# Optimization experiments

Hardware: AMD Instinct MI355X
Metric: run time of the kernel (lower is better)

## Reference

```python
import jax, jax.numpy as jnp
import numpy as np

N_NODES = 50000
N_EDGES = 1600000
D_FEAT = 512
FILTERS = 256
NUM_CLASSES = 16


def setup_inputs() -> dict:
    key = jax.random.key(0)
    k = jax.random.split(key, 6)
    x = jax.random.normal(k[0], (N_NODES, D_FEAT), dtype=jnp.float32)
    W1 = jax.random.normal(k[1], (D_FEAT, FILTERS), dtype=jnp.float32) * (1.0 / np.sqrt(D_FEAT))
    W2 = jax.random.normal(k[2], (FILTERS, NUM_CLASSES), dtype=jnp.float32) * (1.0 / np.sqrt(FILTERS))
    edge_weight = jax.random.uniform(k[3], (N_EDGES,), dtype=jnp.float32)
    edge_src = jax.random.randint(k[4], (N_EDGES,), 0, N_NODES, dtype=jnp.int32)
    edge_dst = jax.random.randint(k[5], (N_EDGES,), 0, N_NODES, dtype=jnp.int32)
    return {"x": x, "W1": W1, "W2": W2, "edge_weight": edge_weight,
            "edge_src": edge_src, "edge_dst": edge_dst}


def _propagate(h, edge_src, edge_dst, edge_weight):
    # sparse A @ h: out[dst] += w * h[src]
    msgs = edge_weight[:, None] * h[edge_src]          # [E, F]
    return jax.ops.segment_sum(msgs, edge_dst, num_segments=N_NODES)


def reference(x, W1, W2, edge_weight, edge_src, edge_dst):
    # Dropout layers are identity at inference (training=False).
    # Layer 1: relu(A @ (X @ W1))
    h = jax.nn.relu(_propagate(x @ W1, edge_src, edge_dst, edge_weight))
    # Layer 2: softmax(A @ (H @ W2))
    logits = _propagate(h @ W2, edge_src, edge_dst, edge_weight)
    return jax.nn.softmax(logits, axis=-1)
```

## Files before the change

### kernel.cpp

```cpp
#include <hip/hip_runtime.h>

#define N_NODES 50000
#define N_EDGES 1600000
#define D_FEAT 512
#define FILTERS 256
#define NUM_CLASSES 16
#define NXCD 8

typedef __bf16 bf16x8 __attribute__((ext_vector_type(8)));
typedef float f32x4 __attribute__((ext_vector_type(4)));
typedef _Float16 half4 __attribute__((ext_vector_type(4)));
typedef _Float16 f16x8 __attribute__((ext_vector_type(8)));

#define GLOAD_LDS16(g, l)                                                  \
  __builtin_amdgcn_global_load_lds(                                        \
      (const __attribute__((address_space(1))) unsigned int*)(g),          \
      (__attribute__((address_space(3))) unsigned int*)(l), 16, 0, 0)

__global__ __launch_bounds__(256) void split_w1_kernel(
    const float* __restrict__ W1, __bf16* __restrict__ Wth,
    __bf16* __restrict__ Wtl) {
  const int idx = blockIdx.x * 256 + threadIdx.x;
  const int k = idx >> 8;
  const int n = idx & 255;
  const float v = W1[idx];
  const __bf16 h = (__bf16)v;
  const __bf16 l = (__bf16)(v - (float)h);
  Wth[n * D_FEAT + k] = h;
  Wtl[n * D_FEAT + k] = l;
}

__global__ __launch_bounds__(256) void hist8_kernel(
    const int* __restrict__ edst, int* __restrict__ deg8) {
  const int e = blockIdx.x * 256 + threadIdx.x;
  if (e >= N_EDGES) return;
  const int x = blockIdx.x & (NXCD - 1);
  atomicAdd(&deg8[x * N_NODES + edst[e]], 1);
}

#define SCAN_NB 196
__global__ __launch_bounds__(256) void scan_blocks_kernel(
    const int* __restrict__ deg8, int* __restrict__ row_ptr,
    int* __restrict__ bsum) {
  __shared__ int s[256];
  const int i = blockIdx.x * 256 + threadIdx.x;
  int v = 0;
  if (i < N_NODES) {
#pragma unroll
    for (int x = 0; x < NXCD; ++x) v += deg8[x * N_NODES + i];
  }
  s[threadIdx.x] = v;
  __syncthreads();
  for (int off = 1; off < 256; off <<= 1) {
    const int t = (threadIdx.x >= off) ? s[threadIdx.x - off] : 0;
    __syncthreads();
    s[threadIdx.x] += t;
    __syncthreads();
  }
  if (i < N_NODES) row_ptr[i] = s[threadIdx.x] - v;
  if (threadIdx.x == 255) bsum[blockIdx.x] = s[255];
}

__global__ __launch_bounds__(256) void scan_sums_kernel(int* __restrict__ bsum) {
  __shared__ int s[256];
  const int v = (threadIdx.x < SCAN_NB) ? bsum[threadIdx.x] : 0;
  s[threadIdx.x] = v;
  __syncthreads();
  for (int off = 1; off < 256; off <<= 1) {
    const int t = (threadIdx.x >= off) ? s[threadIdx.x - off] : 0;
    __syncthreads();
    s[threadIdx.x] += t;
    __syncthreads();
  }
  if (threadIdx.x < SCAN_NB) bsum[threadIdx.x] = s[threadIdx.x] - v;
}

__global__ __launch_bounds__(256) void scan_add_cursor8_kernel(
    int* __restrict__ row_ptr, const int* __restrict__ bsum,
    const int* __restrict__ deg8, int* __restrict__ cursor8) {
  const int i = blockIdx.x * 256 + threadIdx.x;
  if (i < N_NODES) {
    int run = row_ptr[i] + bsum[blockIdx.x];
    row_ptr[i] = run;
#pragma unroll
    for (int x = 0; x < NXCD; ++x) {
      cursor8[x * N_NODES + i] = run;
      run += deg8[x * N_NODES + i];
    }
  }
  if (i == 0) row_ptr[N_NODES] = N_EDGES;
}

__global__ __launch_bounds__(256) void fill8_kernel(
    const int* __restrict__ esrc, const int* __restrict__ edst,
    const float* __restrict__ ew, int* __restrict__ cursor8,
    int4* __restrict__ meta) {
  const int e = blockIdx.x * 256 + threadIdx.x;
  if (e >= N_EDGES) return;
  const int x = blockIdx.x & (NXCD - 1);
  const int d = edst[e];
  const int pos = atomicAdd(&cursor8[x * N_NODES + d], 1);
  meta[pos] = make_int4(esrc[e], __float_as_int(ew[e]), d, 0);
}

__global__ __launch_bounds__(256) void gemm1_mfma_kernel(
    const float* __restrict__ A, const __bf16* __restrict__ Bh,
    const __bf16* __restrict__ Bl, _Float16* __restrict__ C) {
  const int K = D_FEAT;
  __shared__ __bf16 sAh[128 * 32];
  __shared__ __bf16 sAl[128 * 32];
  __shared__ __bf16 sBh[128 * 32];
  __shared__ __bf16 sBl[128 * 32];

  const int tid = threadIdx.x;
  const int wave = tid >> 6;
  const int lane = tid & 63;
  const int wm = (wave >> 1) * 64;
  const int wn = (wave & 1) * 64;
  const int m0 = blockIdx.x * 128;
  const int n0 = blockIdx.y * 128;

  const int arow = tid >> 1;
  const int aks = (tid & 1) * 16;
  int am = m0 + arow;
  if (am >= N_NODES) am = N_NODES - 1;
  const float* aptr = A + (size_t)am * K + aks;

  const int lr = lane >> 2;
  const int lc = (lane & 3) * 8;
  const int fm = lane & 15;
  const int fq = lane >> 4;

  f32x4 acc[4][4] = {};

  for (int k0 = 0; k0 < K; k0 += 32) {
    const float4* ap = (const float4*)(aptr + k0);
    const float4 a0 = ap[0], a1 = ap[1], a2 = ap[2], a3 = ap[3];

    __syncthreads();

#pragma unroll
    for (int i = 0; i < 2; ++i) {
      const int row = wave * 32 + i * 16;
      GLOAD_LDS16(Bh + (size_t)(n0 + row + lr) * K + k0 + lc, sBh + row * 32);
      GLOAD_LDS16(Bl + (size_t)(n0 + row + lr) * K + k0 + lc, sBl + row * 32);
    }

    float va[16] = {a0.x, a0.y, a0.z, a0.w, a1.x, a1.y, a1.z, a1.w,
                    a2.x, a2.y, a2.z, a2.w, a3.x, a3.y, a3.z, a3.w};
    __bf16 hh[16], ll[16];
#pragma unroll
    for (int i = 0; i < 16; ++i) {
      const __bf16 h = (__bf16)va[i];
      hh[i] = h;
      ll[i] = (__bf16)(va[i] - (float)h);
    }
    *(bf16x8*)(sAh + arow * 32 + aks) = *(bf16x8*)&hh[0];
    *(bf16x8*)(sAh + arow * 32 + aks + 8) = *(bf16x8*)&hh[8];
    *(bf16x8*)(sAl + arow * 32 + aks) = *(bf16x8*)&ll[0];
    *(bf16x8*)(sAl + arow * 32 + aks + 8) = *(bf16x8*)&ll[8];

    __syncthreads();

    bf16x8 fah[4], fal[4], fbh[4], fbl[4];
#pragma unroll
    for (int t = 0; t < 4; ++t) {
      const int moff = (wm + t * 16 + fm) * 32 + fq * 8;
      fah[t] = *(const bf16x8*)(sAh + moff);
      fal[t] = *(const bf16x8*)(sAl + moff);
      const int noff = (wn + t * 16 + fm) * 32 + fq * 8;
      fbh[t] = *(const bf16x8*)(sBh + noff);
      fbl[t] = *(const bf16x8*)(sBl + noff);
    }
#pragma unroll
    for (int i = 0; i < 4; ++i)
#pragma unroll
      for (int j = 0; j < 4; ++j)
        acc[i][j] = __builtin_amdgcn_mfma_f32_16x16x32_bf16(fah[i], fbh[j],
                                                            acc[i][j], 0, 0, 0);
#pragma unroll
    for (int i = 0; i < 4; ++i)
#pragma unroll
      for (int j = 0; j < 4; ++j)
        acc[i][j] = __builtin_amdgcn_mfma_f32_16x16x32_bf16(fah[i], fbl[j],
                                                            acc[i][j], 0, 0, 0);
#pragma unroll
    for (int i = 0; i < 4; ++i)
#pragma unroll
      for (int j = 0; j < 4; ++j)
        acc[i][j] = __builtin_amdgcn_mfma_f32_16x16x32_bf16(fal[i], fbh[j],
                                                            acc[i][j], 0, 0, 0);
  }

#pragma unroll
  for (int ti = 0; ti < 4; ++ti) {
#pragma unroll
    for (int r = 0; r < 4; ++r) {
      const int m = m0 + wm + ti * 16 + fq * 4 + r;
      if (m < N_NODES) {
#pragma unroll
        for (int tj = 0; tj < 4; ++tj) {
          const int n = n0 + wn + tj * 16 + fm;
          C[(size_t)m * FILTERS + n] = (_Float16)acc[ti][tj][r];
        }
      }
    }
  }
}

__global__ __launch_bounds__(256) void gather1_gemm2_kernel(
    const _Float16* __restrict__ xw1, const int* __restrict__ row_ptr,
    const int4* __restrict__ meta, const float* __restrict__ W2,
    _Float16* __restrict__ h2) {
  __shared__ float red[4][16][17];
  const int wave = threadIdx.x >> 6;
  const int lane = threadIdx.x & 63;
  const int node = blockIdx.x * 4 + wave;
  const int beg = row_ptr[node];
  const int end = row_ptr[node + 1];

  float acc[4] = {};
  const half4* __restrict__ xw1v = (const half4*)xw1;

  for (int c0 = beg; c0 < end; c0 += 64) {
    const int cnt = min(64, end - c0);
    const int4 mv = meta[c0 + ((lane < cnt) ? lane : 0)];

    for (int j = 0; j < cnt; j += 8) {
      int srcs[8];
      float ws[8];
#pragma unroll
      for (int u = 0; u < 8; ++u) {
        const int live = (j + u < cnt);
        const int l = live ? (j + u) : 0;
        srcs[u] = __builtin_amdgcn_readlane(mv.x, l);
        const int wb = __builtin_amdgcn_readlane(mv.y, l);
        ws[u] = live ? __int_as_float(wb) : 0.f;
      }
      half4 v[8];
#pragma unroll
      for (int u = 0; u < 8; ++u)
        v[u] = xw1v[(unsigned)srcs[u] * 64u + (unsigned)lane];
#pragma unroll
      for (int u = 0; u < 8; ++u)
#pragma unroll
        for (int i = 0; i < 4; ++i)
          acc[i] = fmaf(ws[u], (float)v[u][i], acc[i]);
    }
  }

  float r[4];
#pragma unroll
  for (int i = 0; i < 4; ++i) r[i] = fmaxf(acc[i], 0.f);

  float p[16] = {};
#pragma unroll
  for (int j = 0; j < 4; ++j) {
    const float4* wr = (const float4*)(W2 + (size_t)(lane * 4 + j) * NUM_CLASSES);
#pragma unroll
    for (int c4 = 0; c4 < 4; ++c4) {
      const float4 wv = wr[c4];
      p[c4 * 4 + 0] = fmaf(r[j], wv.x, p[c4 * 4 + 0]);
      p[c4 * 4 + 1] = fmaf(r[j], wv.y, p[c4 * 4 + 1]);
      p[c4 * 4 + 2] = fmaf(r[j], wv.z, p[c4 * 4 + 2]);
      p[c4 * 4 + 3] = fmaf(r[j], wv.w, p[c4 * 4 + 3]);
    }
  }

#pragma unroll
  for (int off = 32; off >= 16; off >>= 1)
#pragma unroll
    for (int i = 0; i < 16; ++i) p[i] += __shfl_xor(p[i], off, 64);

  if (lane < 16) {
#pragma unroll
    for (int i = 0; i < 16; ++i) red[wave][lane][i] = p[i];
  }
  if (lane < 16) {
    float sum = 0.f;
#pragma unroll
    for (int i = 0; i < 16; ++i) sum += red[wave][i][lane];
    h2[(size_t)node * NUM_CLASSES + lane] = (_Float16)sum;
  }
}

__global__ __launch_bounds__(256) void gather2_mfma_kernel(
    const _Float16* __restrict__ h2, const int* __restrict__ row_ptr,
    const int4* __restrict__ meta, float* __restrict__ out) {
  __shared__ _Float16 lds[4][16][72];
  const int wave = threadIdx.x >> 6;
  const int lane = threadIdx.x & 63;
  const int tile = blockIdx.x * 4 + wave;
  if (tile >= N_NODES / 16) return;
  const int t0 = tile * 16;
  const int beg = row_ptr[t0];
  const int end = row_ptr[t0 + 16];

  const int cls = lane & 15;
  const int kq = lane >> 4;
  const int erow = lane >> 1;
  const int part = lane & 1;

  f32x4 acc = {0.f, 0.f, 0.f, 0.f};
  _Float16* myl = &lds[wave][0][0];

  if (beg < end) {
    const int last = end - 1;
    int e = beg + lane;
    int4 m = meta[(e <= last) ? e : last];
    float wv = (e <= last) ? __int_as_float(m.y) : 0.f;

    for (int c0 = beg; c0 < end; c0 += 64) {
      int4 mn = m;
      float wn = 0.f;
      const int c1 = c0 + 64;
      if (c1 < end) {
        const int en = c1 + lane;
        mn = meta[(en <= last) ? en : last];
        wn = (en <= last) ? __int_as_float(mn.y) : 0.f;
      }

      const int se0 = __shfl(m.x, erow, 64);
      const int se1 = __shfl(m.x, 32 + erow, 64);
      const f16x8 r0 =
          *(const f16x8*)(h2 + (size_t)se0 * NUM_CLASSES + part * 8);
      const f16x8 r1 =
          *(const f16x8*)(h2 + (size_t)se1 * NUM_CLASSES + part * 8);

      f16x8 a0, a1;
#pragma unroll
      for (int j = 0; j < 8; ++j) {
        const int ei = kq * 8 + j;
        const int d0 = __shfl(m.z, ei, 64) - t0;
        const float w0 = __shfl(wv, ei, 64);
        a0[j] = (d0 == cls) ? (_Float16)w0 : (_Float16)0.f;
        const int d1 = __shfl(m.z, 32 + ei, 64) - t0;
        const float w1 = __shfl(wv, 32 + ei, 64);
        a1[j] = (d1 == cls) ? (_Float16)w1 : (_Float16)0.f;
      }

#pragma unroll
      for (int j = 0; j < 8; ++j) myl[(part * 8 + j) * 72 + erow] = r0[j];
#pragma unroll
      for (int j = 0; j < 8; ++j) myl[(part * 8 + j) * 72 + 32 + erow] = r1[j];

      const f16x8 b0 = *(const f16x8*)(myl + cls * 72 + kq * 8);
      const f16x8 b1 = *(const f16x8*)(myl + cls * 72 + 32 + kq * 8);

      acc = __builtin_amdgcn_mfma_f32_16x16x32_f16(a0, b0, acc, 0, 0, 0);
      acc = __builtin_amdgcn_mfma_f32_16x16x32_f16(a1, b1, acc, 0, 0, 0);

      m = mn;
      wv = wn;
    }
  }

#pragma unroll
  for (int r = 0; r < 4; ++r) {
    const float a = acc[r];
    float mx = a;
#pragma unroll
    for (int off = 8; off >= 1; off >>= 1)
      mx = fmaxf(mx, __shfl_xor(mx, off, 16));
    const float ex = __expf(a - mx);
    float sm = ex;
#pragma unroll
    for (int off = 8; off >= 1; off >>= 1) sm += __shfl_xor(sm, off, 16);
    out[(size_t)(t0 + kq * 4 + r) * NUM_CLASSES + cls] = ex / sm;
  }
}

extern "C" void kernel_launch(void* const* d_in, const int* in_sizes, int n_in,
                              void* d_out, int out_size, void* d_ws,
                              size_t ws_size, hipStream_t stream) {
  const float* x = (const float*)d_in[0];
  const float* W1 = (const float*)d_in[1];
  const float* W2 = (const float*)d_in[2];
  const float* ew = (const float*)d_in[3];
  const int* esrc = (const int*)d_in[4];
  const int* edst = (const int*)d_in[5];
  float* out = (float*)d_out;

  _Float16* xw1 = (_Float16*)d_ws;
  _Float16* h2 = xw1 + (size_t)N_NODES * FILTERS;
  int* row_ptr = (int*)(h2 + (size_t)N_NODES * NUM_CLASSES);
  int* deg8 = row_ptr + (N_NODES + 1);
  int* cursor8 = deg8 + NXCD * N_NODES;
  int4* meta = (int4*)(((uintptr_t)(cursor8 + NXCD * N_NODES) + 15) &
                       ~(uintptr_t)15);
  __bf16* w1th = (__bf16*)(meta + N_EDGES);
  __bf16* w1tl = w1th + D_FEAT * FILTERS;
  int* bsum = (int*)(w1tl + D_FEAT * FILTERS);

  hipMemsetAsync(deg8, 0, NXCD * N_NODES * sizeof(int), stream);
  hist8_kernel<<<(N_EDGES + 255) / 256, 256, 0, stream>>>(edst, deg8);
  scan_blocks_kernel<<<SCAN_NB, 256, 0, stream>>>(deg8, row_ptr, bsum);
  scan_sums_kernel<<<1, 256, 0, stream>>>(bsum);
  scan_add_cursor8_kernel<<<SCAN_NB, 256, 0, stream>>>(row_ptr, bsum, deg8,
                                                       cursor8);
  fill8_kernel<<<(N_EDGES + 255) / 256, 256, 0, stream>>>(esrc, edst, ew,
                                                          cursor8, meta);

  split_w1_kernel<<<(D_FEAT * FILTERS) / 256, 256, 0, stream>>>(W1, w1th, w1tl);
  dim3 g1((N_NODES + 127) / 128, FILTERS / 128);
  gemm1_mfma_kernel<<<g1, 256, 0, stream>>>(x, w1th, w1tl, xw1);

  gather1_gemm2_kernel<<<N_NODES / 4, 256, 0, stream>>>(xw1, row_ptr, meta, W2,
                                                        h2);

  gather2_mfma_kernel<<<(N_NODES / 16 + 3) / 4, 256, 0, stream>>>(h2, row_ptr,
                                                                  meta, out);
}
```

Measured before the change: 555.8 us.

## Pack edge metadata into 8 bytes and fold small prep kernels

Edge metadata shrinks from an int4 (src, weight, dst, pad) to a uint2. The source index sits in the low 16 bits, the destination's position within its 16-node tile in bits 16-19, and the weight in the second word. This halves metadata traffic in the fill and both gather kernels. The W1 bf16 hi/lo split moves into the block-scan kernel. The separate scan-of-sums kernel is replaced by each block reducing the preceding block sums itself, which removes two launches. The packing relies on node indices fitting in 16 bits.

```diff
diff --git a/kernel.cpp b/kernel.cpp
--- a/kernel.cpp
+++ b/kernel.cpp
@@ -17,19 +17,6 @@
       (const __attribute__((address_space(1))) unsigned int*)(g),          \
       (__attribute__((address_space(3))) unsigned int*)(l), 16, 0, 0)
 
-__global__ __launch_bounds__(256) void split_w1_kernel(
-    const float* __restrict__ W1, __bf16* __restrict__ Wth,
-    __bf16* __restrict__ Wtl) {
-  const int idx = blockIdx.x * 256 + threadIdx.x;
-  const int k = idx >> 8;
-  const int n = idx & 255;
-  const float v = W1[idx];
-  const __bf16 h = (__bf16)v;
-  const __bf16 l = (__bf16)(v - (float)h);
-  Wth[n * D_FEAT + k] = h;
-  Wtl[n * D_FEAT + k] = l;
-}
-
 __global__ __launch_bounds__(256) void hist8_kernel(
     const int* __restrict__ edst, int* __restrict__ deg8) {
   const int e = blockIdx.x * 256 + threadIdx.x;
@@ -41,9 +28,20 @@
 #define SCAN_NB 196
 __global__ __launch_bounds__(256) void scan_blocks_kernel(
     const int* __restrict__ deg8, int* __restrict__ row_ptr,
-    int* __restrict__ bsum) {
+    int* __restrict__ bsum, const float* __restrict__ W1,
+    __bf16* __restrict__ Wth, __bf16* __restrict__ Wtl) {
+  const int gtid = blockIdx.x * 256 + threadIdx.x;
+  for (int i = gtid; i < D_FEAT * FILTERS; i += SCAN_NB * 256) {
+    const float v = W1[i];
+    const int k = i >> 8;
+    const int n = i & 255;
+    const __bf16 h = (__bf16)v;
+    Wth[n * D_FEAT + k] = h;
+    Wtl[n * D_FEAT + k] = (__bf16)(v - (float)h);
+  }
+
   __shared__ int s[256];
-  const int i = blockIdx.x * 256 + threadIdx.x;
+  const int i = gtid;
   int v = 0;
   if (i < N_NODES) {
 #pragma unroll
@@ -61,26 +59,22 @@
   if (threadIdx.x == 255) bsum[blockIdx.x] = s[255];
 }
 
-__global__ __launch_bounds__(256) void scan_sums_kernel(int* __restrict__ bsum) {
-  __shared__ int s[256];
-  const int v = (threadIdx.x < SCAN_NB) ? bsum[threadIdx.x] : 0;
-  s[threadIdx.x] = v;
-  __syncthreads();
-  for (int off = 1; off < 256; off <<= 1) {
-    const int t = (threadIdx.x >= off) ? s[threadIdx.x - off] : 0;
-    __syncthreads();
-    s[threadIdx.x] += t;
-    __syncthreads();
-  }
-  if (threadIdx.x < SCAN_NB) bsum[threadIdx.x] = s[threadIdx.x] - v;
-}
-
 __global__ __launch_bounds__(256) void scan_add_cursor8_kernel(
     int* __restrict__ row_ptr, const int* __restrict__ bsum,
     const int* __restrict__ deg8, int* __restrict__ cursor8) {
+  __shared__ int wsum[4];
+  const int lane = threadIdx.x & 63;
+  const int wave = threadIdx.x >> 6;
+  int v = (threadIdx.x < blockIdx.x) ? bsum[threadIdx.x] : 0;
+#pragma unroll
+  for (int off = 32; off >= 1; off >>= 1) v += __shfl_xor(v, off, 64);
+  if (lane == 0) wsum[wave] = v;
+  __syncthreads();
+  const int boff = wsum[0] + wsum[1] + wsum[2] + wsum[3];
+
   const int i = blockIdx.x * 256 + threadIdx.x;
   if (i < N_NODES) {
-    int run = row_ptr[i] + bsum[blockIdx.x];
+    int run = row_ptr[i] + boff;
     row_ptr[i] = run;
 #pragma unroll
     for (int x = 0; x < NXCD; ++x) {
@@ -94,13 +88,14 @@
 __global__ __launch_bounds__(256) void fill8_kernel(
     const int* __restrict__ esrc, const int* __restrict__ edst,
     const float* __restrict__ ew, int* __restrict__ cursor8,
-    int4* __restrict__ meta) {
+    uint2* __restrict__ meta8) {
   const int e = blockIdx.x * 256 + threadIdx.x;
   if (e >= N_EDGES) return;
   const int x = blockIdx.x & (NXCD - 1);
   const int d = edst[e];
   const int pos = atomicAdd(&cursor8[x * N_NODES + d], 1);
-  meta[pos] = make_int4(esrc[e], __float_as_int(ew[e]), d, 0);
+  meta8[pos] = make_uint2((unsigned)esrc[e] | ((unsigned)(d & 15) << 16),
+                          __float_as_uint(ew[e]));
 }
 
 __global__ __launch_bounds__(256) void gemm1_mfma_kernel(
@@ -210,7 +205,7 @@
 
 __global__ __launch_bounds__(256) void gather1_gemm2_kernel(
     const _Float16* __restrict__ xw1, const int* __restrict__ row_ptr,
-    const int4* __restrict__ meta, const float* __restrict__ W2,
+    const uint2* __restrict__ meta8, const float* __restrict__ W2,
     _Float16* __restrict__ h2) {
   __shared__ float red[4][16][17];
   const int wave = threadIdx.x >> 6;
@@ -224,7 +219,7 @@
 
   for (int c0 = beg; c0 < end; c0 += 64) {
     const int cnt = min(64, end - c0);
-    const int4 mv = meta[c0 + ((lane < cnt) ? lane : 0)];
+    const uint2 mv = meta8[c0 + ((lane < cnt) ? lane : 0)];
 
     for (int j = 0; j < cnt; j += 8) {
       int srcs[8];
@@ -233,8 +228,8 @@
       for (int u = 0; u < 8; ++u) {
         const int live = (j + u < cnt);
         const int l = live ? (j + u) : 0;
-        srcs[u] = __builtin_amdgcn_readlane(mv.x, l);
-        const int wb = __builtin_amdgcn_readlane(mv.y, l);
+        srcs[u] = __builtin_amdgcn_readlane((int)mv.x, l) & 0xFFFF;
+        const int wb = __builtin_amdgcn_readlane((int)mv.y, l);
         ws[u] = live ? __int_as_float(wb) : 0.f;
       }
       half4 v[8];
@@ -286,7 +281,7 @@
 
 __global__ __launch_bounds__(256) void gather2_mfma_kernel(
     const _Float16* __restrict__ h2, const int* __restrict__ row_ptr,
-    const int4* __restrict__ meta, float* __restrict__ out) {
+    const uint2* __restrict__ meta8, float* __restrict__ out) {
   __shared__ _Float16 lds[4][16][72];
   const int wave = threadIdx.x >> 6;
   const int lane = threadIdx.x & 63;
@@ -307,21 +302,21 @@
   if (beg < end) {
     const int last = end - 1;
     int e = beg + lane;
-    int4 m = meta[(e <= last) ? e : last];
-    float wv = (e <= last) ? __int_as_float(m.y) : 0.f;
+    uint2 m = meta8[(e <= last) ? e : last];
+    float wv = (e <= last) ? __uint_as_float(m.y) : 0.f;
 
     for (int c0 = beg; c0 < end; c0 += 64) {
-      int4 mn = m;
+      uint2 mn = m;
       float wn = 0.f;
       const int c1 = c0 + 64;
       if (c1 < end) {
         const int en = c1 + lane;
-        mn = meta[(en <= last) ? en : last];
-        wn = (en <= last) ? __int_as_float(mn.y) : 0.f;
+        mn = meta8[(en <= last) ? en : last];
+        wn = (en <= last) ? __uint_as_float(mn.y) : 0.f;
       }
 
-      const int se0 = __shfl(m.x, erow, 64);
-      const int se1 = __shfl(m.x, 32 + erow, 64);
+      const int se0 = __shfl((int)m.x, erow, 64) & 0xFFFF;
+      const int se1 = __shfl((int)m.x, 32 + erow, 64) & 0xFFFF;
       const f16x8 r0 =
           *(const f16x8*)(h2 + (size_t)se0 * NUM_CLASSES + part * 8);
       const f16x8 r1 =
@@ -331,12 +326,12 @@
 #pragma unroll
       for (int j = 0; j < 8; ++j) {
         const int ei = kq * 8 + j;
-        const int d0 = __shfl(m.z, ei, 64) - t0;
+        const int p0 = __shfl((int)m.x, ei, 64);
         const float w0 = __shfl(wv, ei, 64);
-        a0[j] = (d0 == cls) ? (_Float16)w0 : (_Float16)0.f;
-        const int d1 = __shfl(m.z, 32 + ei, 64) - t0;
+        a0[j] = (((p0 >> 16) & 15) == cls) ? (_Float16)w0 : (_Float16)0.f;
+        const int p1 = __shfl((int)m.x, 32 + ei, 64);
         const float w1 = __shfl(wv, 32 + ei, 64);
-        a1[j] = (d1 == cls) ? (_Float16)w1 : (_Float16)0.f;
+        a1[j] = (((p1 >> 16) & 15) == cls) ? (_Float16)w1 : (_Float16)0.f;
       }
 
 #pragma unroll
@@ -386,28 +381,27 @@
   int* row_ptr = (int*)(h2 + (size_t)N_NODES * NUM_CLASSES);
   int* deg8 = row_ptr + (N_NODES + 1);
   int* cursor8 = deg8 + NXCD * N_NODES;
-  int4* meta = (int4*)(((uintptr_t)(cursor8 + NXCD * N_NODES) + 15) &
-                       ~(uintptr_t)15);
-  __bf16* w1th = (__bf16*)(meta + N_EDGES);
+  uint2* meta8 = (uint2*)(((uintptr_t)(cursor8 + NXCD * N_NODES) + 15) &
+                          ~(uintptr_t)15);
+  __bf16* w1th = (__bf16*)(meta8 + N_EDGES);
   __bf16* w1tl = w1th + D_FEAT * FILTERS;
   int* bsum = (int*)(w1tl + D_FEAT * FILTERS);
 
   hipMemsetAsync(deg8, 0, NXCD * N_NODES * sizeof(int), stream);
   hist8_kernel<<<(N_EDGES + 255) / 256, 256, 0, stream>>>(edst, deg8);
-  scan_blocks_kernel<<<SCAN_NB, 256, 0, stream>>>(deg8, row_ptr, bsum);
-  scan_sums_kernel<<<1, 256, 0, stream>>>(bsum);
+  scan_blocks_kernel<<<SCAN_NB, 256, 0, stream>>>(deg8, row_ptr, bsum, W1,
+                                                  w1th, w1tl);
   scan_add_cursor8_kernel<<<SCAN_NB, 256, 0, stream>>>(row_ptr, bsum, deg8,
                                                        cursor8);
   fill8_kernel<<<(N_EDGES + 255) / 256, 256, 0, stream>>>(esrc, edst, ew,
-                                                          cursor8, meta);
-
-  split_w1_kernel<<<(D_FEAT * FILTERS) / 256, 256, 0, stream>>>(W1, w1th, w1tl);
+                                                          cursor8, meta8);
+
   dim3 g1((N_NODES + 127) / 128, FILTERS / 128);
   gemm1_mfma_kernel<<<g1, 256, 0, stream>>>(x, w1th, w1tl, xw1);
 
-  gather1_gemm2_kernel<<<N_NODES / 4, 256, 0, stream>>>(xw1, row_ptr, meta, W2,
-                                                        h2);
+  gather1_gemm2_kernel<<<N_NODES / 4, 256, 0, stream>>>(xw1, row_ptr, meta8,
+                                                        W2, h2);
 
   gather2_mfma_kernel<<<(N_NODES / 16 + 3) / 4, 256, 0, stream>>>(h2, row_ptr,
-                                                                  meta, out);
-}
+                                                                  meta8, out);
+}
```

New measurement: 544.6 us. 2.0% less time.
